# Kernel tuning notes

Measured on AMD Instinct MI355X. Metric: run time of the kernel, lower is better.

## Reference

```python
import jax, jax.numpy as jnp
from jax import lax
import numpy as np

T, B, I, H, O = 512, 64, 512, 1024, 512


def setup_inputs() -> dict:
    key = jax.random.key(0)
    ks = jax.random.split(key, 8)
    s_ih = 1.0 / np.sqrt(I)
    s_hh = 1.0 / np.sqrt(H)
    return {
        "x": jax.random.normal(ks[0], (T, B, I), dtype=jnp.float32),
        "hidden": jnp.zeros((1, B, H), dtype=jnp.float32),
        "W_ih": jax.random.normal(ks[1], (H, I), dtype=jnp.float32) * s_ih,
        "W_hh": jax.random.normal(ks[2], (H, H), dtype=jnp.float32) * s_hh,
        "b_ih": jax.random.normal(ks[3], (H,), dtype=jnp.float32) * s_hh,
        "b_hh": jax.random.normal(ks[4], (H,), dtype=jnp.float32) * s_hh,
        "W_fc": jax.random.normal(ks[5], (O, H), dtype=jnp.float32) * s_hh,
        "b_fc": jax.random.normal(ks[6], (O,), dtype=jnp.float32) * s_hh,
    }


def reference(x, hidden, W_ih, W_hh, b_ih, b_hh, W_fc, b_fc):
    # Precompute the input projection for all timesteps as one big GEMM.
    # xp: [T, B, H]
    xp = jnp.einsum("tbi,hi->tbh", x, W_ih) + b_ih

    h0 = hidden[0]  # [B, H]

    def step(h, xt):
        # PyTorch RNN (tanh): h_t = tanh(W_ih x_t + b_ih + W_hh h_{t-1} + b_hh)
        h_new = jnp.tanh(xt + h @ W_hh.T + b_hh)
        return h_new, h_new

    h_last, hs = lax.scan(step, h0, xp)  # hs: [T, B, H]

    # fc applied to flattened [T*B, H] hidden states
    out = hs.reshape(-1, hs.shape[-1]) @ W_fc.T + b_fc  # [T*B, O]
    return out, h_last[None]  # ([T*B, O], [1, B, H])
```

## Files before the change

### kernel.cpp

```cpp
#include <hip/hip_runtime.h>

typedef __attribute__((ext_vector_type(8))) short bf16x8;
typedef __attribute__((ext_vector_type(4))) float f32x4;

#define T_N 512
#define I_N 512
#define H_N 1024
#define O_N 512
#define NCL 4
#define NMEM 16
#define NTHR 512
#define COLS_H 64
#define KW 192
#define AP_STRIDE 1544
#define RST 9
#define CANARY 0xFFFFFFFFu
#define HS_CAP 20000000
#define POLL_CAP 200000

__device__ __forceinline__ unsigned short f2bf(float f) {
  unsigned int u = __float_as_uint(f);
  u += 0x7fffu + ((u >> 16) & 1u);
  return (unsigned short)(u >> 16);
}
__device__ __forceinline__ bf16x8 cvt8f(const float* __restrict__ p) {
  float4 a = *(const float4*)p;
  float4 b = *(const float4*)(p + 4);
  bf16x8 r;
  r[0] = (short)f2bf(a.x); r[1] = (short)f2bf(a.y);
  r[2] = (short)f2bf(a.z); r[3] = (short)f2bf(a.w);
  r[4] = (short)f2bf(b.x); r[5] = (short)f2bf(b.y);
  r[6] = (short)f2bf(b.z); r[7] = (short)f2bf(b.w);
  return r;
}
__device__ __forceinline__ bf16x8 cvt8v(float4 a, float4 b) {
  bf16x8 r;
  r[0] = (short)f2bf(a.x); r[1] = (short)f2bf(a.y);
  r[2] = (short)f2bf(a.z); r[3] = (short)f2bf(a.w);
  r[4] = (short)f2bf(b.x); r[5] = (short)f2bf(b.y);
  r[6] = (short)f2bf(b.z); r[7] = (short)f2bf(b.w);
  return r;
}

__device__ __forceinline__ void st_sc01(unsigned int* p, unsigned int v) {
  asm volatile("global_store_dword %0, %1, off sc0 sc1" :: "v"(p), "v"(v) : "memory");
}
__device__ __forceinline__ unsigned int ld_sc01(const unsigned int* p) {
  unsigned int r;
  asm volatile("global_load_dword %0, %1, off sc0 sc1\n\ts_waitcnt vmcnt(0)"
               : "=v"(r) : "v"(p) : "memory");
  return r;
}
__device__ __forceinline__ void ld4_sc01(uint4* d, const void* p) {
  asm volatile("global_load_dwordx4 %0, %1, off sc0 sc1" : "=v"(*d) : "v"(p) : "memory");
}
__device__ __forceinline__ void ld4_rawf(float4* d, const void* p) {
  asm volatile("global_load_dwordx4 %0, %1, off" : "=v"(*d) : "v"(p) : "memory");
}
__device__ __forceinline__ bool has_canary(uint4 a, uint4 b) {
  return (a.x == CANARY) | (a.y == CANARY) | (a.z == CANARY) | (a.w == CANARY) |
         (b.x == CANARY) | (b.y == CANARY) | (b.z == CANARY) | (b.w == CANARY);
}

#define PHASE(G, X0, X1, X2, X3)                                               \
  {                                                                            \
    f32x4 acc0 = {}, acc1 = {}, acc2 = {}, acc3 = {};                          \
    const int abase = (l & 15) * AP_STRIDE + wv * KW + ((l >> 4) << 3);        \
    _Pragma("unroll")                                                          \
    for (int kst = 0; kst < 6; ++kst) {                                        \
      bf16x8 a = *(const bf16x8*)(Apan + abase + kst * 32);                    \
      acc0 = __builtin_amdgcn_mfma_f32_16x16x32_bf16(a, Bh[kst][0], acc0,0,0,0);\
      acc1 = __builtin_amdgcn_mfma_f32_16x16x32_bf16(a, Bh[kst][1], acc1,0,0,0);\
      acc2 = __builtin_amdgcn_mfma_f32_16x16x32_bf16(a, Bh[kst][2], acc2,0,0,0);\
      acc3 = __builtin_amdgcn_mfma_f32_16x16x32_bf16(a, Bh[kst][3], acc3,0,0,0);\
    }                                                                          \
    if ((l >> 5) == (G)) {            \
      const int rb = ((l >> 4) & 1) << 2;                                      \
      *(f32x4*)(R + (size_t)(wv * COLS_H +  0 + (l & 15)) * RST + rb) = acc0;  \
      *(f32x4*)(R + (size_t)(wv * COLS_H + 16 + (l & 15)) * RST + rb) = acc1;  \
      *(f32x4*)(R + (size_t)(wv * COLS_H + 32 + (l & 15)) * RST + rb) = acc2;  \
      *(f32x4*)(R + (size_t)(wv * COLS_H + 48 + (l & 15)) * RST + rb) = acc3;  \
    }                                                                          \
    __syncthreads();                                                           \
    if (wv < 4) {                                                              \
      float v0 = pb0, v1 = pb1;                                                \
      _Pragma("unroll")                                                        \
      for (int kk = 0; kk < 8; ++kk) {                                         \
        v0 += R[(size_t)(kk * COLS_H + 2 * rcp)     * RST + rrow];             \
        v1 += R[(size_t)(kk * COLS_H + 2 * rcp + 1) * RST + rrow];             \
      }                                                                        \
      const float h0 = tanhf(v0), h1 = tanhf(v1);                              \
      const unsigned int pk =                                                  \
          (unsigned int)f2bf(h0) | ((unsigned int)f2bf(h1) << 16);             \
      st_sc01(ringc + ((G) * 4 + (t & 3)) * 4096 + pubdw, pk);                 \
      st_sc01(ringc + ((G) * 4 + ((t + 2) & 3)) * 4096 + pubdw, CANARY);       \
      *(unsigned int*)(hs + ((size_t)t * 64 + b0 + (G) * 8 + rrow) * H_N +     \
                       cbh + 2 * rcp) = pk;                                    \
      if (t == T_N - 1) {                                                      \
        float2 fv; fv.x = h0; fv.y = h1;                                       \
        *(float2*)(hlast + (size_t)(b0 + (G) * 8 + rrow) * H_N + cbh + 2 * rcp) = fv; \
      }                                                                        \
    } else if (t + 1 < T_N) {                  \
      asm volatile("s_waitcnt vmcnt(0)" ::: "memory");                         \
      const int u = tid & 255;                                                 \
      *(bf16x8*)(Apan + ((G) * 8 + (u >> 6)) * AP_STRIDE + H_N + ((u & 63) << 3)) = \
          cvt8v(X0, X1);                                                       \
      *(bf16x8*)(Apan + ((G) * 8 + (u >> 6) + 4) * AP_STRIDE + H_N + ((u & 63) << 3)) = \
          cvt8v(X2, X3);                                                       \
    }                                                                          \
    if (!((G) == 0 && t == 0)) {          \
      const int swt = t - 1 + (G);                                             \
      const unsigned int* sl = ringc + (((G) ^ 1) * 4 + (swt & 3)) * 4096;     \
      const uint4* sp = (const uint4*)sl + (tid << 1);                         \
      uint4 u0, u1; int it = 0;                                                \
      while (true) {                                                           \
        ld4_sc01(&u0, sp); ld4_sc01(&u1, sp + 1);                              \
        asm volatile("s_waitcnt vmcnt(0)" ::: "memory");                       \
        if (!has_canary(u0, u1) || ++it >= POLL_CAP) break;                    \
        __builtin_amdgcn_s_sleep(1);                                           \
      }                                                                        \
      const int prow = (((G) ^ 1) * 8) + (tid >> 6), pcol = (tid & 63) << 4;   \
      *(uint4*)(Apan + prow * AP_STRIDE + pcol)     = u0;                      \
      *(uint4*)(Apan + prow * AP_STRIDE + pcol + 8) = u1;                      \
    }                                                                          \
    if (wv >= 4 && t + 2 < T_N) {                      \
      const int u = tid & 255;                                                 \
      const float* px = x + ((size_t)(t + 2) * 64 + b0 + (G) * 8 + (u >> 6)) * I_N + \
                        ((u & 63) << 3);                                       \
      ld4_rawf(&X0, px); ld4_rawf(&X1, px + 4);                                \
      ld4_rawf(&X2, px + 4 * I_N); ld4_rawf(&X3, px + 4 * I_N + 4);            \
    }                                                                          \
    __syncthreads();                                                           \
  }

__global__ __launch_bounds__(NTHR, 2) void rnn_scan(
    const float* __restrict__ x, const float* __restrict__ hidden,
    const float* __restrict__ Wih, const float* __restrict__ Whh,
    const float* __restrict__ bih, const float* __restrict__ bhh,
    unsigned short* __restrict__ hs, float* __restrict__ hlast,
    unsigned int* __restrict__ ring, unsigned int* __restrict__ flags)
{
  __shared__ __align__(16) unsigned short Apan[16 * AP_STRIDE];
  __shared__ __align__(16) float R[8 * COLS_H * RST];

  const int tid = threadIdx.x;
  const int l = tid & 63, wv = tid >> 6;
  const int bid = blockIdx.x;
  const int c = bid & 3;
  const int m = bid >> 2;
  const int b0 = c * 16;
  const int cbh = m * COLS_H;
  unsigned int* ringc = ring + (size_t)c * 2 * 4 * 4096;
  unsigned int* bar = flags + c * 64;

  bf16x8 Bh[6][4];
  {
    const int kb0 = wv * KW + ((l >> 4) << 3);
#pragma unroll
    for (int kst = 0; kst < 6; ++kst) {
      const int k = kb0 + kst * 32;
#pragma unroll
      for (int f = 0; f < 4; ++f) {
        const int col = cbh + f * 16 + (l & 15);
        const float* src = (k < H_N) ? (Whh + (size_t)col * H_N + k)
                                     : (Wih + (size_t)col * I_N + (k - H_N));
        Bh[kst][f] = cvt8f(src);
      }
    }
  }
  const int rrow = (tid >> 5) & 7;
  const int rcp  = tid & 31;
  const float pb0 = bih[cbh + 2 * rcp]     + bhh[cbh + 2 * rcp];
  const float pb1 = bih[cbh + 2 * rcp + 1] + bhh[cbh + 2 * rcp + 1];
  const int pubdw = rrow * 512 + m * 32 + rcp;

  {
    int q = tid;
#pragma unroll
    for (int i = 0; i < 4; ++i, q += NTHR) {
      const int row = q >> 7, col8 = (q & 127) << 3;
      *(bf16x8*)(Apan + row * AP_STRIDE + col8) =
          cvt8f(hidden + (size_t)(b0 + row) * H_N + col8);
    }
  }
  {
    int q = tid;
#pragma unroll
    for (int i = 0; i < 2; ++i, q += NTHR) {
      const int row = q >> 6, col8 = (q & 63) << 3;
      *(bf16x8*)(Apan + row * AP_STRIDE + H_N + col8) =
          cvt8f(x + (size_t)(b0 + row) * I_N + col8);
    }
  }
  if (tid < 256) {
#pragma unroll
    for (int s = 0; s < 8; ++s) st_sc01(ringc + s * 4096 + pubdw, CANARY);
  }
  asm volatile("s_waitcnt vmcnt(0)" ::: "memory");
  __syncthreads();
  if (tid == 0) st_sc01(&bar[m], 1u);
  if (tid < NMEM) {
    int it = 0;
    while (ld_sc01(&bar[tid]) < 1u && ++it < HS_CAP)
      if (it > 64) __builtin_amdgcn_s_sleep(1);
  }
  float4 xA0, xA1, xA2, xA3, xB0, xB1, xB2, xB3;
  if (wv >= 4) {
    const int u = tid & 255;
    const float* pa = x + (size_t)(64 + b0 + (u >> 6)) * I_N + ((u & 63) << 3);
    ld4_rawf(&xA0, pa); ld4_rawf(&xA1, pa + 4);
    ld4_rawf(&xA2, pa + 4 * I_N); ld4_rawf(&xA3, pa + 4 * I_N + 4);
    const float* pb = x + (size_t)(64 + b0 + 8 + (u >> 6)) * I_N + ((u & 63) << 3);
    ld4_rawf(&xB0, pb); ld4_rawf(&xB1, pb + 4);
    ld4_rawf(&xB2, pb + 4 * I_N); ld4_rawf(&xB3, pb + 4 * I_N + 4);
  }
  __syncthreads();

  for (int t = 0; t < T_N; ++t) {
    PHASE(0, xA0, xA1, xA2, xA3)
    PHASE(1, xB0, xB1, xB2, xB3)
  }
}

__global__ __launch_bounds__(256) void gemm_fc(const unsigned short* __restrict__ A,
                                               const unsigned short* __restrict__ Bt,
                                               const float* __restrict__ bias,
                                               float* __restrict__ C) {
  const int N = O_N, K = H_N;
  const int bm = blockIdx.x >> 2, bn = blockIdx.x & 3;
  const int l = threadIdx.x & 63, w = threadIdx.x >> 6;
  const int wr = w >> 1, wc = w & 1;
  const int row_a = bm * 128 + wr * 64 + (l & 15);
  const int row_b = bn * 128 + wc * 64 + (l & 15);
  const int koff = (l >> 4) * 8;
  f32x4 acc[4][4] = {};
  for (int k = 0; k < K; k += 32) {
    bf16x8 a[4], b[4];
#pragma unroll
    for (int i = 0; i < 4; i++)
      a[i] = *(const bf16x8*)(A + (size_t)(row_a + i * 16) * K + k + koff);
#pragma unroll
    for (int i = 0; i < 4; i++)
      b[i] = *(const bf16x8*)(Bt + (size_t)(row_b + i * 16) * K + k + koff);
#pragma unroll
    for (int i = 0; i < 4; i++)
#pragma unroll
      for (int j = 0; j < 4; j++)
        acc[i][j] = __builtin_amdgcn_mfma_f32_16x16x32_bf16(a[i], b[j], acc[i][j], 0, 0, 0);
  }
  const int orow = bm * 128 + wr * 64 + ((l >> 4) << 2);
  const int ocol = bn * 128 + wc * 64 + (l & 15);
#pragma unroll
  for (int i = 0; i < 4; i++)
#pragma unroll
    for (int j = 0; j < 4; j++) {
      const int r0 = orow + i * 16, c0 = ocol + j * 16;
      const float bv = bias[c0];
#pragma unroll
      for (int r = 0; r < 4; r++)
        C[(size_t)(r0 + r) * N + c0] = acc[i][j][r] + bv;
    }
}

__global__ __launch_bounds__(256) void cvt8(const float* __restrict__ s,
                                            unsigned short* __restrict__ d, long n) {
  long i = ((long)blockIdx.x * blockDim.x + threadIdx.x) * 8;
  if (i < n) *(bf16x8*)(d + i) = cvt8f(s + i);
}

extern "C" void kernel_launch(void* const* d_in, const int* in_sizes, int n_in,
                              void* d_out, int out_size, void* d_ws, size_t ws_size,
                              hipStream_t stream) {
  const float* x   = (const float*)d_in[0];
  const float* hid = (const float*)d_in[1];
  const float* Wih = (const float*)d_in[2];
  const float* Whh = (const float*)d_in[3];
  const float* bih = (const float*)d_in[4];
  const float* bhh = (const float*)d_in[5];
  const float* Wfc = (const float*)d_in[6];
  const float* bfc = (const float*)d_in[7];

  float* out   = (float*)d_out;
  float* hlast = out + (size_t)32768 * 512;

  unsigned int*   flags = (unsigned int*)d_ws;
  unsigned int*   ring  = (unsigned int*)((char*)d_ws + 4096);
  unsigned short* Wfcb  = (unsigned short*)((char*)d_ws + 4096 + 524288);
  unsigned short* hsb   = Wfcb + (size_t)512 * 1024;

  hipMemsetAsync(flags, 0, 4096, stream);
  cvt8<<<256, 256, 0, stream>>>(Wfc, Wfcb, (long)512 * 1024);
  rnn_scan<<<64, NTHR, 0, stream>>>(x, hid, Wih, Whh, bih, bhh, hsb, hlast, ring, flags);
  gemm_fc<<<1024, 256, 0, stream>>>(hsb, Wfcb, bfc, out);
}
```

Measured before the change: 1.699 ms.

## Issue ring sweep loads before MFMA phase to overlap cross-block exchange latency

The polling loads that fetch the neighbouring half's hidden state from the global ring are now issued at the start of each phase, before the MFMA compute, so their latency overlaps with the matrix work. The loads become per-dword coalesced reads into registers that are checked for the canary after the compute and re-polled only if still stale, then written to LDS. The x prefetch wait is relaxed to partial vmcnt counts, and the sweep is skipped on the final G=1 step. This adds register pressure and fragile vmcnt bookkeeping, and it risks reading stale data early, which then costs a re-poll.

```diff
diff --git a/kernel.cpp b/kernel.cpp
--- a/kernel.cpp
+++ b/kernel.cpp
@@ -45,25 +45,40 @@
 __device__ __forceinline__ void st_sc01(unsigned int* p, unsigned int v) {
   asm volatile("global_store_dword %0, %1, off sc0 sc1" :: "v"(p), "v"(v) : "memory");
 }
+__device__ __forceinline__ void st_raw32(unsigned int* p, unsigned int v) {
+  asm volatile("global_store_dword %0, %1, off" :: "v"(p), "v"(v) : "memory");
+}
 __device__ __forceinline__ unsigned int ld_sc01(const unsigned int* p) {
   unsigned int r;
   asm volatile("global_load_dword %0, %1, off sc0 sc1\n\ts_waitcnt vmcnt(0)"
                : "=v"(r) : "v"(p) : "memory");
   return r;
 }
-__device__ __forceinline__ void ld4_sc01(uint4* d, const void* p) {
-  asm volatile("global_load_dwordx4 %0, %1, off sc0 sc1" : "=v"(*d) : "v"(p) : "memory");
+__device__ __forceinline__ void ld_sc01_rw(unsigned int* d, const unsigned int* p) {
+  asm volatile("global_load_dword %0, %1, off sc0 sc1" : "+v"(*d) : "v"(p) : "memory");
+}
+__device__ __forceinline__ void ld_sc01_nw(unsigned int* d, const unsigned int* p) {
+  asm volatile("global_load_dword %0, %1, off sc0 sc1" : "=v"(*d) : "v"(p) : "memory");
 }
 __device__ __forceinline__ void ld4_rawf(float4* d, const void* p) {
   asm volatile("global_load_dwordx4 %0, %1, off" : "=v"(*d) : "v"(p) : "memory");
 }
-__device__ __forceinline__ bool has_canary(uint4 a, uint4 b) {
-  return (a.x == CANARY) | (a.y == CANARY) | (a.z == CANARY) | (a.w == CANARY) |
-         (b.x == CANARY) | (b.y == CANARY) | (b.z == CANARY) | (b.w == CANARY);
-}
 
 #define PHASE(G, X0, X1, X2, X3)                                               \
   {                                                                            \
+    const bool doSweep = !((G) == 0 && t == 0) && !((G) == 1 && t == T_N - 1); \
+    unsigned int sw[8];                                                        \
+    const unsigned int* spd = ringc;                                           \
+    if (doSweep) {                                                             \
+      const int swt = t - 1 + (G);                                             \
+      spd = ringc + (((G) ^ 1) * 4 + (swt & 3)) * 4096 + tid;                  \
+      _Pragma("unroll")                                                        \
+      for (int j = 0; j < 8; ++j) {                                            \
+        sw[j] = CANARY;                                                        \
+        ld_sc01_rw(&sw[j], spd + 512 * j);                                     \
+      }                                                                        \
+    }                                                                          \
+                     \
     f32x4 acc0 = {}, acc1 = {}, acc2 = {}, acc3 = {};                          \
     const int abase = (l & 15) * AP_STRIDE + wv * KW + ((l >> 4) << 3);        \
     _Pragma("unroll")                                                          \
@@ -74,7 +89,7 @@
       acc2 = __builtin_amdgcn_mfma_f32_16x16x32_bf16(a, Bh[kst][2], acc2,0,0,0);\
       acc3 = __builtin_amdgcn_mfma_f32_16x16x32_bf16(a, Bh[kst][3], acc3,0,0,0);\
     }                                                                          \
-    if ((l >> 5) == (G)) {            \
+    if ((l >> 5) == (G)) {      \
       const int rb = ((l >> 4) & 1) << 2;                                      \
       *(f32x4*)(R + (size_t)(wv * COLS_H +  0 + (l & 15)) * RST + rb) = acc0;  \
       *(f32x4*)(R + (size_t)(wv * COLS_H + 16 + (l & 15)) * RST + rb) = acc1;  \
@@ -92,43 +107,78 @@
       const float h0 = tanhf(v0), h1 = tanhf(v1);                              \
       const unsigned int pk =                                                  \
           (unsigned int)f2bf(h0) | ((unsigned int)f2bf(h1) << 16);             \
+                             \
       st_sc01(ringc + ((G) * 4 + (t & 3)) * 4096 + pubdw, pk);                 \
       st_sc01(ringc + ((G) * 4 + ((t + 2) & 3)) * 4096 + pubdw, CANARY);       \
-      *(unsigned int*)(hs + ((size_t)t * 64 + b0 + (G) * 8 + rrow) * H_N +     \
-                       cbh + 2 * rcp) = pk;                                    \
+      st_raw32((unsigned int*)(hs + ((size_t)t * 64 + b0 + (G) * 8 + rrow) * H_N \
+                               + cbh + 2 * rcp), pk);                          \
+      if (doSweep) {                                                           \
+        asm volatile("s_waitcnt vmcnt(3)" ::: "memory");   \
+        __builtin_amdgcn_sched_barrier(0);                                     \
+        bool bad = false;                                                      \
+        _Pragma("unroll")                                                      \
+        for (int j = 0; j < 8; ++j) bad |= (sw[j] == CANARY);                  \
+        if (bad) {                                                             \
+          int it = 0;                                                          \
+          do {                                                                 \
+            _Pragma("unroll")                                                  \
+            for (int j = 0; j < 8; ++j) ld_sc01_nw(&sw[j], spd + 512 * j);     \
+            asm volatile("s_waitcnt vmcnt(0)" ::: "memory");                   \
+            __builtin_amdgcn_sched_barrier(0);                                 \
+            bad = false;                                                       \
+            _Pragma("unroll")                                                  \
+            for (int j = 0; j < 8; ++j) bad |= (sw[j] == CANARY);              \
+          } while (bad && ++it < POLL_CAP);                                    \
+        }                                                                      \
+      }                                                                        \
       if (t == T_N - 1) {                                                      \
         float2 fv; fv.x = h0; fv.y = h1;                                       \
         *(float2*)(hlast + (size_t)(b0 + (G) * 8 + rrow) * H_N + cbh + 2 * rcp) = fv; \
       }                                                                        \
-    } else if (t + 1 < T_N) {                  \
-      asm volatile("s_waitcnt vmcnt(0)" ::: "memory");                         \
-      const int u = tid & 255;                                                 \
-      *(bf16x8*)(Apan + ((G) * 8 + (u >> 6)) * AP_STRIDE + H_N + ((u & 63) << 3)) = \
-          cvt8v(X0, X1);                                                       \
-      *(bf16x8*)(Apan + ((G) * 8 + (u >> 6) + 4) * AP_STRIDE + H_N + ((u & 63) << 3)) = \
-          cvt8v(X2, X3);                                                       \
-    }                                                                          \
-    if (!((G) == 0 && t == 0)) {          \
-      const int swt = t - 1 + (G);                                             \
-      const unsigned int* sl = ringc + (((G) ^ 1) * 4 + (swt & 3)) * 4096;     \
-      const uint4* sp = (const uint4*)sl + (tid << 1);                         \
-      uint4 u0, u1; int it = 0;                                                \
-      while (true) {                                                           \
-        ld4_sc01(&u0, sp); ld4_sc01(&u1, sp + 1);                              \
+    } else {                                                                   \
+      if (t == 0) {    \
+        if ((G) == 0) asm volatile("s_waitcnt vmcnt(4)" ::: "memory");         \
+        else          asm volatile("s_waitcnt vmcnt(8)" ::: "memory");         \
+        __builtin_amdgcn_sched_barrier(0);                                     \
+      }   \
+      if (t + 1 < T_N) {                                                       \
+        const int u = tid & 255;                                               \
+        *(bf16x8*)(Apan + ((G) * 8 + (u >> 6)) * AP_STRIDE + H_N + ((u & 63) << 3)) = \
+            cvt8v(X0, X1);                                                     \
+        *(bf16x8*)(Apan + ((G) * 8 + (u >> 6) + 4) * AP_STRIDE + H_N + ((u & 63) << 3)) = \
+            cvt8v(X2, X3);                                                     \
+      }                                                                        \
+      if (doSweep) {                                                           \
         asm volatile("s_waitcnt vmcnt(0)" ::: "memory");                       \
-        if (!has_canary(u0, u1) || ++it >= POLL_CAP) break;                    \
-        __builtin_amdgcn_s_sleep(1);                                           \
-      }                                                                        \
-      const int prow = (((G) ^ 1) * 8) + (tid >> 6), pcol = (tid & 63) << 4;   \
-      *(uint4*)(Apan + prow * AP_STRIDE + pcol)     = u0;                      \
-      *(uint4*)(Apan + prow * AP_STRIDE + pcol + 8) = u1;                      \
-    }                                                                          \
-    if (wv >= 4 && t + 2 < T_N) {                      \
-      const int u = tid & 255;                                                 \
-      const float* px = x + ((size_t)(t + 2) * 64 + b0 + (G) * 8 + (u >> 6)) * I_N + \
-                        ((u & 63) << 3);                                       \
-      ld4_rawf(&X0, px); ld4_rawf(&X1, px + 4);                                \
-      ld4_rawf(&X2, px + 4 * I_N); ld4_rawf(&X3, px + 4 * I_N + 4);            \
+        __builtin_amdgcn_sched_barrier(0);                                     \
+        bool bad = false;                                                      \
+        _Pragma("unroll")                                                      \
+        for (int j = 0; j < 8; ++j) bad |= (sw[j] == CANARY);                  \
+        if (bad) {                                                             \
+          int it = 0;                                                          \
+          do {                                                                 \
+            _Pragma("unroll")                                                  \
+            for (int j = 0; j < 8; ++j) ld_sc01_nw(&sw[j], spd + 512 * j);     \
+            asm volatile("s_waitcnt vmcnt(0)" ::: "memory");                   \
+            __builtin_amdgcn_sched_barrier(0);                                 \
+            bad = false;                                                       \
+            _Pragma("unroll")                                                  \
+            for (int j = 0; j < 8; ++j) bad |= (sw[j] == CANARY);              \
+          } while (bad && ++it < POLL_CAP);                                    \
+        }                                                                      \
+      }                                                                        \
+      if (t + 2 < T_N) {    \
+        const int u = tid & 255;                                               \
+        const float* px = x + ((size_t)(t + 2) * 64 + b0 + (G) * 8 + (u >> 6)) * I_N \
+                          + ((u & 63) << 3);                                   \
+        ld4_rawf(&X0, px); ld4_rawf(&X1, px + 4);                              \
+        ld4_rawf(&X2, px + 4 * I_N); ld4_rawf(&X3, px + 4 * I_N + 4);          \
+      }                                                                        \
+    }                                                                          \
+    if (doSweep) {     \
+      _Pragma("unroll")                                                        \
+      for (int j = 0; j < 8; ++j)                                              \
+        *(unsigned int*)(Apan + ((((G) ^ 1) * 8) + j) * AP_STRIDE + (tid << 1)) = sw[j]; \
     }                                                                          \
     __syncthreads();                                                           \
   }
@@ -288,7 +338,7 @@
   unsigned short* Wfcb  = (unsigned short*)((char*)d_ws + 4096 + 524288);
   unsigned short* hsb   = Wfcb + (size_t)512 * 1024;
 
-  hipMemsetAsync(flags, 0, 4096, stream);
+  (void)hipMemsetAsync(flags, 0, 4096, stream);
   cvt8<<<256, 256, 0, stream>>>(Wfc, Wfcb, (long)512 * 1024);
   rnn_scan<<<64, NTHR, 0, stream>>>(x, hid, Wih, Whh, bih, bhh, hsb, hlast, ring, flags);
   gemm_fc<<<1024, 256, 0, stream>>>(hsb, Wfcb, bfc, out);
```

After: 1.694 ms. About the same (-0.3%).
